# Kernel tuning notes

Hardware: AMD Instinct MI355X
Metric: run time of the kernel (lower is better)

Reference implementation:

```python
import jax, jax.numpy as jnp
import numpy as np

NUM_HEADS = 8
DIM = 384
KSIZE = 9  # res_kernel_size


def _moe_fc(x2d, gate_w, gate_b, w0, b0, w1, b1):
    # NaiveGate with top_k=1: softmax over a single top-1 logit == 1.0, so the
    # SparseDispatcher dispatch/exp/mul/log combine reduces exactly to selecting
    # the argmax expert's output per token.
    logits = x2d @ gate_w + gate_b                      # [T, 2]
    sel = jnp.argmax(logits, axis=-1)[:, None]          # [T, 1]
    y0 = x2d @ w0.T + b0
    y1 = x2d @ w1.T + b1
    return jnp.where(sel == 0, y0, y1)


def _forward(x, qkv_gate_w, qkv_gate_b, qkv_w0, qkv_w1,
             proj_gate_w, proj_gate_b, proj_w0, proj_b0, proj_w1, proj_b1,
             dconv_w):
    B, N, C = x.shape
    h, hd = NUM_HEADS, C // NUM_HEADS
    xt = x.reshape(-1, C)
    zero3 = jnp.zeros((3 * C,), x.dtype)  # qkv_bias=False
    qkv = _moe_fc(xt, qkv_gate_w, qkv_gate_b, qkv_w0, zero3, qkv_w1, zero3)
    qkv = qkv.reshape(B, N, 3, h, hd).transpose(2, 0, 3, 1, 4)  # [3,B,h,N,d]
    q, k, v = qkv[0], qkv[1], qkv[2]

    q = q / jnp.linalg.norm(q, axis=-1, keepdims=True)
    k = k / jnp.linalg.norm(k, axis=-1, keepdims=True)
    scale1 = jnp.mean(jnp.abs(q))
    scale2 = jnp.mean(jnp.abs(k))
    # straight-through binarization: fwd value = (x>0)*scale, grad flows via clamp(x,0,1)
    cq = jnp.clip(q, 0.0, 1.0)
    q = jax.lax.stop_gradient((q > 0).astype(q.dtype) * scale1 - cq) + cq
    ck = jnp.clip(k, 0.0, 1.0)
    k = jax.lax.stop_gradient((k > 0).astype(k.dtype) * scale2 - ck) + ck

    # depthwise residual conv over the token axis: v is [B, h, N, d], kernel (9,1)
    dconv_v = jax.lax.conv_general_dilated(
        v, dconv_w, window_strides=(1, 1), padding=[(KSIZE // 2, KSIZE // 2), (0, 0)],
        feature_group_count=h, dimension_numbers=("NCHW", "OIHW", "NCHW"))

    # linear-attention reorder: (K^T V) first -> O(N d^2)
    attn = jnp.einsum("bhnd,bhne->bhde", k, v)          # [B,h,d,d]
    out = 0.5 * v - (1.0 / jnp.pi) * jnp.einsum("bhnd,bhde->bhne", q, attn)
    out = out / jnp.linalg.norm(out, axis=-1, keepdims=True)
    out = out + dconv_v
    out = out.transpose(0, 2, 1, 3).reshape(B, N, C)

    out = _moe_fc(out.reshape(-1, C), proj_gate_w, proj_gate_b,
                  proj_w0, proj_b0, proj_w1, proj_b1)
    return out.reshape(B, N, C)


def setup_inputs() -> dict:
    key = jax.random.key(0)
    ks = jax.random.split(key, 12)
    B, N, C = 8, 4096, DIM
    s = 0.02
    return {
        "x": jax.random.normal(ks[0], (B, N, C), jnp.float32),
        "H": 64,
        "W": 64,
        "qkv_gate_w": jax.random.normal(ks[1], (C, 2), jnp.float32) * s,
        "qkv_gate_b": jnp.zeros((2,), jnp.float32),
        "qkv_w0": jax.random.normal(ks[2], (3 * C, C), jnp.float32) * s,
        "qkv_w1": jax.random.normal(ks[3], (3 * C, C), jnp.float32) * s,
        "proj_gate_w": jax.random.normal(ks[4], (C, 2), jnp.float32) * s,
        "proj_gate_b": jnp.zeros((2,), jnp.float32),
        "proj_w0": jax.random.normal(ks[5], (C, C), jnp.float32) * s,
        "proj_b0": jnp.zeros((C,), jnp.float32),
        "proj_w1": jax.random.normal(ks[6], (C, C), jnp.float32) * s,
        "proj_b1": jnp.zeros((C,), jnp.float32),
        "dconv_w": jax.random.normal(ks[7], (NUM_HEADS, 1, KSIZE, 1), jnp.float32) * s,
    }


def reference(x, H, W, qkv_gate_w, qkv_gate_b, qkv_w0, qkv_w1,
              proj_gate_w, proj_gate_b, proj_w0, proj_b0, proj_w1, proj_b1,
              dconv_w):
    # H, W are unused by the math (kept for signature fidelity)
    return _forward(x, qkv_gate_w, qkv_gate_b, qkv_w0, qkv_w1,
                    proj_gate_w, proj_gate_b, proj_w0, proj_b0, proj_w1, proj_b1,
                    dconv_w)
```

## Files before the change

### kernel.cpp

```cpp
#include <hip/hip_runtime.h>
#include <hip/hip_bf16.h>

#define BB 8
#define NN 4096
#define CC 384
#define HH 8
#define DD 48
#define TT (BB*NN)
#define CAP (TT + 128)
#define NROWT (CAP/128)
#define NQ ((size_t)BB*HH*NN*DD)
#define LISTCAP 32768

static_assert(CAP % 128 == 0, "cap");

typedef __attribute__((ext_vector_type(8))) short bf16x8;
typedef __attribute__((ext_vector_type(4))) float f32x4;

__device__ __forceinline__ float waveRedSum(float v){
  #pragma unroll
  for (int o = 32; o > 0; o >>= 1) v += __shfl_xor(v, o);
  return v;
}

__device__ __forceinline__ unsigned short f2bf(float f){
  unsigned u = __float_as_uint(f);
  u += 0x7FFFu + ((u >> 16) & 1u);
  return (unsigned short)(u >> 16);
}
__device__ __forceinline__ float bf2f(unsigned short h){
  return __uint_as_float(((unsigned)h) << 16);
}

__global__ void k_setup(const float* __restrict__ qw0, const float* __restrict__ qw1,
                        const float* __restrict__ pw0, const float* __restrict__ pw1,
                        unsigned short* __restrict__ qw0h, unsigned short* __restrict__ qw0l,
                        unsigned short* __restrict__ qw1h, unsigned short* __restrict__ qw1l,
                        unsigned short* __restrict__ pw0h, unsigned short* __restrict__ pw0l,
                        unsigned short* __restrict__ pw1h, unsigned short* __restrict__ pw1l,
                        int* __restrict__ perm0, int* __restrict__ perm1, int* __restrict__ cur){
  const int NQW = 1152*384/4, NPW = 384*384/4;
  if (blockIdx.x >= 1152){
    int i = (blockIdx.x - 1152)*256 + threadIdx.x;
    if (i < 8) cur[i] = 0;
    if (i < CAP){ perm0[i] = -1; perm1[i] = -1; }
    return;
  }
  int i = blockIdx.x*256 + threadIdx.x;
  const float* src; unsigned short* hi; unsigned short* lo; int off;
  if (i < NQW){ src = qw0; hi = qw0h; lo = qw0l; off = i; }
  else if (i < 2*NQW){ src = qw1; hi = qw1h; lo = qw1l; off = i - NQW; }
  else if (i < 2*NQW + NPW){ src = pw0; hi = pw0h; lo = pw0l; off = i - 2*NQW; }
  else if (i < 2*NQW + 2*NPW){ src = pw1; hi = pw1h; lo = pw1l; off = i - 2*NQW - NPW; }
  else return;
  float4 v = ((const float4*)src)[off];
  float f[4] = {v.x, v.y, v.z, v.w};
  unsigned short h[4], l[4];
  #pragma unroll
  for (int j = 0; j < 4; j++){
    h[j] = f2bf(f[j]);
    l[j] = f2bf(f[j] - bf2f(h[j]));
  }
  uint2 hv, lv;
  hv.x = h[0] | ((unsigned)h[1] << 16); hv.y = h[2] | ((unsigned)h[3] << 16);
  lv.x = l[0] | ((unsigned)l[1] << 16); lv.y = l[2] | ((unsigned)l[3] << 16);
  ((uint2*)hi)[off] = hv;
  ((uint2*)lo)[off] = lv;
}

__global__ void k_gate_scatter(const float* __restrict__ X,
                               const float* __restrict__ gw, const float* __restrict__ gb,
                               int* __restrict__ perm, int* __restrict__ cur,
                               unsigned char* __restrict__ selb,
                               unsigned short* __restrict__ Xhi, unsigned short* __restrict__ Xlo){
  const int lane = threadIdx.x & 63;
  const int wave = threadIdx.x >> 6;
  float gd[6];
  #pragma unroll
  for (int j = 0; j < 6; j++){
    int c = lane + 64*j;
    gd[j] = gw[c*2+1] - gw[c*2];
  }
  const float gbd = gb[1] - gb[0];
  const int tok0 = (blockIdx.x*4 + wave) * 32;
  unsigned mask = 0u;
  for (int i = 0; i < 32; i++){
    const size_t rowoff = (size_t)(tok0 + i) * CC;
    const float* xr = X + rowoff;
    float d = 0.f;
    #pragma unroll
    for (int j = 0; j < 6; j++){
      float xv = xr[lane + 64*j];
      d = fmaf(xv, gd[j], d);
      unsigned short h = f2bf(xv);
      Xhi[rowoff + lane + 64*j] = h;
      Xlo[rowoff + lane + 64*j] = f2bf(xv - bf2f(h));
    }
    d = waveRedSum(d);
    if (d + gbd > 0.f) mask |= (1u << i);
  }
  int n1 = __popc(mask), n0 = 32 - n1;
  int b0 = 0, b1 = 0;
  if (lane == 0){
    b0 = atomicAdd(cur + 0, n0);
    b1 = atomicAdd(cur + 1, n1);
  }
  b0 = __shfl(b0, 0); b1 = __shfl(b1, 0);
  if (lane < 32){
    int sel = (mask >> lane) & 1;
    unsigned below = mask & ((1u << lane) - 1u);
    int r1 = __popc(below);
    int r0 = lane - r1;
    int idx = sel ? (CAP - 1 - (b1 + r1)) : (b0 + r0);
    perm[idx] = tok0 + lane;
    selb[tok0 + lane] = (unsigned char)sel;
  }
}

__global__ void k_gate2(const float* __restrict__ gpart, const float* __restrict__ gb,
                        int* __restrict__ perm, int* __restrict__ cur){
  const int t = blockIdx.x*256 + threadIdx.x;
  const int lane = threadIdx.x & 63;
  const float gbd = gb[1] - gb[0];
  float4 a = ((const float4*)(gpart + (size_t)t*8))[0];
  float4 c = ((const float4*)(gpart + (size_t)t*8))[1];
  float d = ((a.x + a.y) + (a.z + a.w)) + ((c.x + c.y) + (c.z + c.w)) + gbd;
  bool sel = d > 0.f;
  unsigned long long m = __ballot(sel);
  int n1 = (int)__popcll(m);
  int b0 = 0, b1 = 0;
  if (lane == 0){
    b0 = atomicAdd(cur + 0, 64 - n1);
    b1 = atomicAdd(cur + 1, n1);
  }
  b0 = __shfl(b0, 0); b1 = __shfl(b1, 0);
  unsigned long long below = m & ((1ull << lane) - 1ull);
  int r1 = (int)__popcll(below);
  int r0 = lane - r1;
  int idx = sel ? (CAP - 1 - (b1 + r1)) : (b0 + r0);
  perm[idx] = t;
}

template<int NCOLS, int PASSES, bool IS_QKV>
__global__ __launch_bounds__(256, 2)
void k_gemm_mfma(const unsigned short* __restrict__ Ahi_g, const unsigned short* __restrict__ Alo_g,
                 const unsigned short* __restrict__ W0h, const unsigned short* __restrict__ W0l,
                 const unsigned short* __restrict__ W1h, const unsigned short* __restrict__ W1l,
                 const float* __restrict__ bias0, const float* __restrict__ bias1,
                 const int* __restrict__ perm, const int* __restrict__ cur,
                 unsigned short* __restrict__ oq, unsigned short* __restrict__ ok,
                 float* __restrict__ ov, float* __restrict__ oproj,
                 int* __restrict__ tlist, int* __restrict__ tcnt)
{
  constexpr int GDX = NCOLS / 128;
  constexpr int NWG = GDX * NROWT;
  constexpr int NB = (PASSES == 3) ? 2 : 1;
  __shared__ unsigned short As[NB][128*32];
  __shared__ unsigned short Bs[NB][128*32];
  __shared__ int permv[128];

  int orig = blockIdx.y * GDX + blockIdx.x;
  constexpr int qq = NWG >> 3, rr = NWG & 7;
  int xcd = orig & 7, slot = orig >> 3;
  int logical = (xcd < rr) ? (xcd*(qq+1) + slot) : (rr*(qq+1) + (xcd-rr)*qq + slot);
  const int bx = logical % GDX, by = logical / GDX;

  const int tid = threadIdx.x;
  const int m0 = by * 128, n0 = bx * 128;
  if (tid < 128) permv[tid] = perm[m0 + tid];
  __syncthreads();
  const int expert = (m0 > cur[0]) ? 1 : 0;
  const unsigned short* Wh = expert ? W1h : W0h;
  const unsigned short* Wl = expert ? W1l : W0l;

  const int c0 = tid, c1 = tid + 256;
  const int r0 = c0 >> 2, r1 = c1 >> 2;
  const int s0 = (((c0 & 3) ^ ((r0 >> 1) & 3))) * 8;
  const int s1 = (((c1 & 3) ^ ((r1 >> 1) & 3))) * 8;
  int t0 = permv[r0]; if (t0 < 0) t0 = 0;
  int t1 = permv[r1]; if (t1 < 0) t1 = 0;
  const unsigned short* a0h = Ahi_g + (size_t)t0*CC + s0;
  const unsigned short* a1h = Ahi_g + (size_t)t1*CC + s1;
  const unsigned short* b0h = Wh + (size_t)(n0 + r0)*CC + s0;
  const unsigned short* b1h = Wh + (size_t)(n0 + r1)*CC + s1;
  const unsigned short* a0l = nullptr; const unsigned short* a1l = nullptr;
  const unsigned short* b0l = nullptr; const unsigned short* b1l = nullptr;
  if constexpr (PASSES == 3){
    a0l = Alo_g + (size_t)t0*CC + s0;
    a1l = Alo_g + (size_t)t1*CC + s1;
    b0l = Wl + (size_t)(n0 + r0)*CC + s0;
    b1l = Wl + (size_t)(n0 + r1)*CC + s1;
  }
  const int d0 = c0*8, d1 = c1*8;

  const int lane = tid & 63;
  const int wv = tid >> 6, wr = wv >> 1, wc2 = wv & 1;
  const int lr = lane & 15, lg = lane >> 4;

  f32x4 acc[4][4];
  #pragma unroll
  for (int i = 0; i < 4; i++)
    #pragma unroll
    for (int j = 0; j < 4; j++) acc[i][j] = (f32x4){0.f, 0.f, 0.f, 0.f};

  int aoff[4], boff[4];
  #pragma unroll
  for (int f = 0; f < 4; f++){
    int ra = wr*64 + f*16 + lr;
    aoff[f] = ra*32 + ((lg ^ ((ra >> 1) & 3)) * 8);
    int rb = wc2*64 + f*16 + lr;
    boff[f] = rb*32 + ((lg ^ ((rb >> 1) & 3)) * 8);
  }

  #define GLD(gp, lp) __builtin_amdgcn_global_load_lds( \
      (const __attribute__((address_space(1))) void*)(gp), \
      (__attribute__((address_space(3))) void*)(lp), 16, 0, 0)

  for (int ko = 0; ko < CC; ko += 32){
    GLD(a0h + ko, &As[0][d0]);
    GLD(a1h + ko, &As[0][d1]);
    GLD(b0h + ko, &Bs[0][d0]);
    GLD(b1h + ko, &Bs[0][d1]);
    if constexpr (PASSES == 3){
      GLD(a0l + ko, &As[1][d0]);
      GLD(a1l + ko, &As[1][d1]);
      GLD(b0l + ko, &Bs[1][d0]);
      GLD(b1l + ko, &Bs[1][d1]);
    }
    __syncthreads();
    bf16x8 ah[4], bh[4], al[4], bl[4];
    #pragma unroll
    for (int f = 0; f < 4; f++){
      ah[f] = *(const bf16x8*)&As[0][aoff[f]];
      bh[f] = *(const bf16x8*)&Bs[0][boff[f]];
      if constexpr (PASSES == 3){
        al[f] = *(const bf16x8*)&As[1][aoff[f]];
        bl[f] = *(const bf16x8*)&Bs[1][boff[f]];
      }
    }
    #pragma unroll
    for (int mf = 0; mf < 4; mf++)
      #pragma unroll
      for (int nf = 0; nf < 4; nf++){
        acc[mf][nf] = __builtin_amdgcn_mfma_f32_16x16x32_bf16(ah[mf], bh[nf], acc[mf][nf], 0, 0, 0);
        if constexpr (PASSES == 3){
          acc[mf][nf] = __builtin_amdgcn_mfma_f32_16x16x32_bf16(al[mf], bh[nf], acc[mf][nf], 0, 0, 0);
          acc[mf][nf] = __builtin_amdgcn_mfma_f32_16x16x32_bf16(ah[mf], bl[nf], acc[mf][nf], 0, 0, 0);
        }
      }
    __syncthreads();
  }
  #undef GLD

  #pragma unroll
  for (int mf = 0; mf < 4; mf++){
    #pragma unroll
    for (int j = 0; j < 4; j++){
      const int rl = wr*64 + mf*16 + lg*4 + j;
      const int t = permv[rl];
      if (t < 0) continue;
      const int b = t >> 12, nn = t & 4095;
      #pragma unroll
      for (int nf = 0; nf < 4; nf++){
        const int col = n0 + wc2*64 + nf*16 + lr;
        const float val = acc[mf][nf][j];
        if constexpr (IS_QKV){
          const int which = col / CC;
          const int rem = col - which*CC;
          const int h = rem / DD;
          const int e = rem - h*DD;
          const size_t off = (((size_t)b*HH + h)*NN + nn)*DD + e;
          if (which == 0){
            oq[off] = f2bf(val);
            if (fabsf(val) < 2.5e-5f){
              int pq = atomicAdd(tcnt, 1);
              if (pq < LISTCAP) tlist[pq] = (int)off;
            }
          } else if (which == 1){
            ok[off] = f2bf(val);
            if (fabsf(val) < 2.5e-5f){
              int pq = atomicAdd(tcnt, 1);
              if (pq < LISTCAP) tlist[pq] = (int)(off + NQ);
            }
          } else {
            ov[off] = val;
          }
        } else {
          const float* bs = expert ? bias1 : bias0;
          oproj[(size_t)t*CC + col] = val + bs[col];
        }
      }
    }
  }
}

__global__ void k_topup_scales(unsigned short* __restrict__ qb, unsigned short* __restrict__ kb,
                               const int* __restrict__ list, const int* __restrict__ cnt,
                               const float* __restrict__ x,
                               const float* __restrict__ w0, const float* __restrict__ w1,
                               const unsigned char* __restrict__ selb,
                               float* __restrict__ part){
  __shared__ float sq[256], sk[256];
  if (blockIdx.x < 64){
    const int lane = threadIdx.x & 63;
    const int gw = (blockIdx.x*256 + threadIdx.x) >> 6;
    const int nwaves = 64 * 4;
    int n = cnt[0]; if (n > LISTCAP) n = LISTCAP;
    for (int e = gw; e < n; e += nwaves){
      int idx = list[e];
      int isK = (idx >= (int)NQ);
      int li = isK ? idx - (int)NQ : idx;
      int d = li % DD; int rest = li / DD;
      int nn = rest & 4095; int bh = rest >> 12;
      int b = bh >> 3, h = bh & 7;
      int t = b*NN + nn;
      int col = (isK ? CC : 0) + h*DD + d;
      const float* w = selb[t] ? w1 : w0;
      const float* xr = x + (size_t)t*CC;
      const float* wr = w + (size_t)col*CC;
      float s = 0.f;
      #pragma unroll
      for (int j = 0; j < 6; j++) s = fmaf(xr[lane + 64*j], wr[lane + 64*j], s);
      s = waveRedSum(s);
      if (lane == 0) (isK ? kb : qb)[li] = f2bf(s);
    }
    return;
  }
  const int blk = blockIdx.x - 64;
  const int row = blk*256 + threadIdx.x;
  const uint4* qp = (const uint4*)(qb + (size_t)row*DD);
  const uint4* kp = (const uint4*)(kb + (size_t)row*DD);
  float qss = 0.f, qsa = 0.f, kss = 0.f, ksa = 0.f;
  #pragma unroll
  for (int j = 0; j < 6; j++){
    uint4 u = qp[j];
    unsigned w[4] = {u.x, u.y, u.z, u.w};
    #pragma unroll
    for (int q2 = 0; q2 < 4; q2++){
      float f0 = bf2f((unsigned short)(w[q2] & 0xFFFFu));
      float f1 = bf2f((unsigned short)(w[q2] >> 16));
      qss = fmaf(f0, f0, qss); qsa += fabsf(f0);
      qss = fmaf(f1, f1, qss); qsa += fabsf(f1);
    }
    uint4 v = kp[j];
    unsigned w2[4] = {v.x, v.y, v.z, v.w};
    #pragma unroll
    for (int q2 = 0; q2 < 4; q2++){
      float f0 = bf2f((unsigned short)(w2[q2] & 0xFFFFu));
      float f1 = bf2f((unsigned short)(w2[q2] >> 16));
      kss = fmaf(f0, f0, kss); ksa += fabsf(f0);
      kss = fmaf(f1, f1, kss); ksa += fabsf(f1);
    }
  }
  sq[threadIdx.x] = qsa / sqrtf(qss);
  sk[threadIdx.x] = ksa / sqrtf(kss);
  __syncthreads();
  for (int s = 128; s > 0; s >>= 1){
    if (threadIdx.x < s){ sq[threadIdx.x] += sq[threadIdx.x+s]; sk[threadIdx.x] += sk[threadIdx.x+s]; }
    __syncthreads();
  }
  if (threadIdx.x == 0){
    part[blk*2+0] = sq[0];
    part[blk*2+1] = sk[0];
  }
}

__global__ void k_sred_attnp(const float* __restrict__ part_in, float* __restrict__ scalesb,
                             const unsigned short* __restrict__ kb, const float* __restrict__ vb,
                             float* __restrict__ part_out){
  if (blockIdx.x == 0){
    __shared__ float sq[256], sk[256];
    const int t = threadIdx.x;
    float aq = 0.f, ak = 0.f;
    for (int i = t; i < 1024; i += 256){ aq += part_in[2*i]; ak += part_in[2*i+1]; }
    sq[t] = aq; sk[t] = ak;
    __syncthreads();
    for (int s = 128; s > 0; s >>= 1){
      if (t < s){ sq[t] += sq[t+s]; sk[t] += sk[t+s]; }
      __syncthreads();
    }
    if (t == 0){
      scalesb[0] = sq[0] * (1.0f/12582912.0f);
      scalesb[1] = sk[0] * (1.0f/12582912.0f);
    }
    return;
  }
  __shared__ float ks[64][48];
  __shared__ float vs[64][48];
  const int idx = blockIdx.x - 1;
  const int bh = idx & 63, seg = idx >> 6;
  const int tid = threadIdx.x;
  const int ti = tid >> 5;
  const int tj = (tid >> 2) & 7;
  const int sl = tid & 3;
  const int dd0 = ti*6, ee0 = tj*6;
  const unsigned short* kbase = kb + ((size_t)bh*NN + seg*512) * DD;
  const float* vbase = vb + ((size_t)bh*NN + seg*512) * DD;
  float acc[6][6] = {};
  for (int c = 0; c < 8; c++){
    __syncthreads();
    for (int f = tid*2; f < 3072; f += 512){
      unsigned kk2 = *(const unsigned*)(kbase + c*3072 + f);
      float2 vv2 = *(const float2*)(vbase + c*3072 + f);
      (&ks[0][0])[f]   = ((short)(unsigned short)(kk2 & 0xFFFFu) > 0) ? 1.f : 0.f;
      (&ks[0][0])[f+1] = ((short)(unsigned short)(kk2 >> 16) > 0) ? 1.f : 0.f;
      (&vs[0][0])[f]   = vv2.x;
      (&vs[0][0])[f+1] = vv2.y;
    }
    __syncthreads();
    for (int nl = sl*16; nl < sl*16 + 16; nl++){
      float kk[6], vv[6];
      #pragma unroll
      for (int i = 0; i < 6; i++){ kk[i] = ks[nl][dd0+i]; vv[i] = vs[nl][ee0+i]; }
      #pragma unroll
      for (int i = 0; i < 6; i++)
        #pragma unroll
        for (int j = 0; j < 6; j++)
          acc[i][j] = fmaf(kk[i], vv[j], acc[i][j]);
    }
  }
  float* p = part_out + ((size_t)seg*64 + bh) * (DD*DD);
  #pragma unroll
  for (int i = 0; i < 6; i++)
    #pragma unroll
    for (int j = 0; j < 6; j++){
      float a = acc[i][j];
      a += __shfl_xor(a, 1);
      a += __shfl_xor(a, 2);
      if (sl == 0) p[(dd0+i)*48 + (ee0+j)] = a;
    }
}

__global__ void k_attn_reduce(const float* __restrict__ part, const float* __restrict__ scalesb,
                              unsigned short* __restrict__ aTh, unsigned short* __restrict__ aTl){
  const int bh = blockIdx.x;
  const float s2 = scalesb[1];
  for (int f = threadIdx.x; f < 3072; f += 256){
    const int e = f >> 6, d = f & 63;
    float s = 0.f;
    if (d < 48){
      #pragma unroll
      for (int seg = 0; seg < 8; seg++) s += part[((size_t)seg*64 + bh)*2304 + d*48 + e];
      s *= s2;
    }
    unsigned short hi = f2bf(s);
    aTh[(size_t)bh*3072 + f] = hi;
    aTl[(size_t)bh*3072 + f] = f2bf(s - bf2f(hi));
  }
}

__global__ __launch_bounds__(256, 4)
void k_fused(const unsigned short* __restrict__ qb, const float* __restrict__ vb,
             const unsigned short* __restrict__ aTh, const unsigned short* __restrict__ aTl,
             const float* __restrict__ scalesb, const float* __restrict__ dw,
             const float* __restrict__ pgw,
             unsigned short* __restrict__ intermh, float* __restrict__ gpart){
  __shared__ unsigned short aT[2][48*72];
  __shared__ float S_lds[128*48];
  __shared__ float wc[16];
  const int chunk = blockIdx.x;
  const int bh = blockIdx.y;
  const int b = bh >> 3, h = bh & 7;
  const int tid = threadIdx.x;
  const int lane = tid & 63, w = tid >> 6;
  const int lr = lane & 15, lg = lane >> 4;

  for (int idx = tid; idx < 384; idx += 256){
    const int e = idx >> 3, sl = idx & 7;
    *(uint4*)&aT[0][e*72 + sl*8] = *(const uint4*)(aTh + (size_t)bh*3072 + e*64 + sl*8);
    *(uint4*)&aT[1][e*72 + sl*8] = *(const uint4*)(aTl + (size_t)bh*3072 + e*64 + sl*8);
  }
  if (tid < 9) wc[tid] = dw[h*9 + tid];
  __syncthreads();

  bf16x8 afr[2][2];
  #pragma unroll
  for (int m = 0; m < 2; m++){
    #pragma unroll
    for (int ks = 0; ks < 2; ks++){
      const int d0 = ks*32 + lg*8;
      bf16x8 a = (bf16x8){0,0,0,0,0,0,0,0};
      if (d0 < 48){
        const int tok = chunk*128 + (w*2+m)*16 + lr;
        uint4 raw = *(const uint4*)(qb + ((size_t)bh*NN + tok)*DD + d0);
        unsigned wd[4] = {raw.x, raw.y, raw.z, raw.w};
        #pragma unroll
        for (int i2 = 0; i2 < 8; i2++){
          unsigned short el = (unsigned short)((wd[i2 >> 1] >> ((i2 & 1)*16)) & 0xFFFFu);
          a[i2] = ((short)el > 0) ? (short)0x3F80 : (short)0;
        }
      }
      afr[m][ks] = a;
    }
  }
  f32x4 acc[2][3];
  #pragma unroll
  for (int m = 0; m < 2; m++)
    #pragma unroll
    for (int nf = 0; nf < 3; nf++) acc[m][nf] = (f32x4){0.f,0.f,0.f,0.f};
  #pragma unroll
  for (int nf = 0; nf < 3; nf++){
    bf16x8 bhv[2], blv[2];
    #pragma unroll
    for (int ks = 0; ks < 2; ks++){
      const int bo = (nf*16 + lr)*72 + ks*32 + lg*8;
      bhv[ks] = *(const bf16x8*)&aT[0][bo];
      blv[ks] = *(const bf16x8*)&aT[1][bo];
    }
    #pragma unroll
    for (int m = 0; m < 2; m++)
      #pragma unroll
      for (int ks = 0; ks < 2; ks++){
        acc[m][nf] = __builtin_amdgcn_mfma_f32_16x16x32_bf16(afr[m][ks], bhv[ks], acc[m][nf], 0, 0, 0);
        acc[m][nf] = __builtin_amdgcn_mfma_f32_16x16x32_bf16(afr[m][ks], blv[ks], acc[m][nf], 0, 0, 0);
      }
  }
  #pragma unroll
  for (int m = 0; m < 2; m++)
    #pragma unroll
    for (int nf = 0; nf < 3; nf++)
      #pragma unroll
      for (int j = 0; j < 4; j++)
        S_lds[((w*2+m)*16 + lg*4 + j)*48 + nf*16 + lr] = acc[m][nf][j];
  __syncthreads();

  const float coef = scalesb[0] * 0.31830988618379067f;
  const float gdh = (lane < 48) ? (pgw[(h*48+lane)*2+1] - pgw[(h*48+lane)*2]) : 0.f;
  const float* vrow = vb + (size_t)bh*NN*DD;
  const int n0 = chunk*128 + w*32;
  float ring[9];
  #pragma unroll
  for (int k2 = 0; k2 < 8; k2++){
    int nn2 = n0 - 4 + k2;
    ring[k2] = (nn2 >= 0 && nn2 < NN && lane < 48) ? vrow[(size_t)nn2*DD + lane] : 0.f;
  }
  for (int it = 0; it < 32; it++){
    const int n = n0 + it;
    const int nh = n + 4;
    ring[8] = (nh < NN && lane < 48) ? vrow[(size_t)nh*DD + lane] : 0.f;
    const float vv = ring[4];
    const float Sv = (lane < 48) ? S_lds[(w*32 + it)*48 + lane] : 0.f;
    float op = 0.5f*vv - coef*Sv;
    float ss = waveRedSum(op*op);
    float res = op / sqrtf(ss);
    float dc = 0.f;
    #pragma unroll
    for (int k2 = 0; k2 < 9; k2++) dc = fmaf(wc[k2], ring[k2], dc);
    float r = res + dc;
    if (lane < 48)
      intermh[((size_t)b*NN + n)*CC + h*DD + lane] = f2bf(r);
    float gp = waveRedSum(r*gdh);
    if (lane == 0) gpart[((size_t)b*NN + n)*8 + h] = gp;
    #pragma unroll
    for (int k2 = 0; k2 < 8; k2++) ring[k2] = ring[k2+1];
  }
}

extern "C" void kernel_launch(void* const* d_in, const int* in_sizes, int n_in,
                              void* d_out, int out_size, void* d_ws, size_t ws_size,
                              hipStream_t stream){
  const float* x    = (const float*)d_in[0];
  const float* qgw  = (const float*)d_in[3];
  const float* qgb  = (const float*)d_in[4];
  const float* qw0  = (const float*)d_in[5];
  const float* qw1  = (const float*)d_in[6];
  const float* pgw  = (const float*)d_in[7];
  const float* pgb  = (const float*)d_in[8];
  const float* pw0  = (const float*)d_in[9];
  const float* pb0  = (const float*)d_in[10];
  const float* pw1  = (const float*)d_in[11];
  const float* pb1  = (const float*)d_in[12];
  const float* dw   = (const float*)d_in[13];
  float* out = (float*)d_out;

  char* p = (char*)d_ws;
  auto alloc = [&](size_t bytes){ char* r = p; p += (bytes + 255) & ~(size_t)255; return r; };

  unsigned short* qbuf = (unsigned short*)alloc(2*NQ);
  unsigned short* kbuf = (unsigned short*)alloc(2*NQ);
  float* vbuf          = (float*)alloc(4*NQ);
  char* xreg           = alloc(4*NQ);
  unsigned short* Xhi  = (unsigned short*)xreg;
  unsigned short* Xlo  = Xhi + NQ;
  unsigned short* intermh = (unsigned short*)xreg;
  unsigned short* qw0h = (unsigned short*)alloc(2*1152*384);
  unsigned short* qw0l = (unsigned short*)alloc(2*1152*384);
  unsigned short* qw1h = (unsigned short*)alloc(2*1152*384);
  unsigned short* qw1l = (unsigned short*)alloc(2*1152*384);
  unsigned short* pw0h = (unsigned short*)alloc(2*384*384);
  unsigned short* pw0l = (unsigned short*)alloc(2*384*384);
  unsigned short* pw1h = (unsigned short*)alloc(2*384*384);
  unsigned short* pw1l = (unsigned short*)alloc(2*384*384);
  float* attn_part     = (float*)alloc(4*(size_t)8*64*2304);
  unsigned short* aTh  = (unsigned short*)alloc(2*(size_t)64*3072);
  unsigned short* aTl  = (unsigned short*)alloc(2*(size_t)64*3072);
  float* scale_part    = (float*)alloc(4*2048);
  float* scalesb       = (float*)alloc(64);
  float* gpart         = (float*)alloc(4*(size_t)TT*8);
  int* perm_qkv        = (int*)alloc(4*CAP);
  int* perm_proj       = (int*)alloc(4*CAP);
  int* cur             = (int*)alloc(64);
  int* list            = (int*)alloc(4*LISTCAP);
  unsigned char* selq  = (unsigned char*)alloc(TT);

  k_setup<<<1152 + (CAP + 255)/256, 256, 0, stream>>>(
      qw0, qw1, pw0, pw1,
      qw0h, qw0l, qw1h, qw1l, pw0h, pw0l, pw1h, pw1l,
      perm_qkv, perm_proj, cur);

  k_gate_scatter<<<256, 256, 0, stream>>>(x, qgw, qgb, perm_qkv, cur, selq, Xhi, Xlo);

  {
    dim3 g(9, NROWT);
    k_gemm_mfma<1152, 3, true><<<g, 256, 0, stream>>>(
        Xhi, Xlo, qw0h, qw0l, qw1h, qw1l, nullptr, nullptr,
        perm_qkv, cur, qbuf, kbuf, vbuf, nullptr, list, cur + 4);
  }

  k_topup_scales<<<64 + 1024, 256, 0, stream>>>(qbuf, kbuf, list, cur + 4,
                                                x, qw0, qw1, selq, scale_part);

  k_sred_attnp<<<1 + 512, 256, 0, stream>>>(scale_part, scalesb, kbuf, vbuf, attn_part);

  k_attn_reduce<<<64, 256, 0, stream>>>(attn_part, scalesb, aTh, aTl);

  {
    dim3 g(32, 64);
    k_fused<<<g, 256, 0, stream>>>(qbuf, vbuf, aTh, aTl, scalesb, dw, pgw, intermh, gpart);
  }

  k_gate2<<<TT/256, 256, 0, stream>>>(gpart, pgb, perm_proj, cur + 2);

  {
    dim3 g(3, NROWT);
    k_gemm_mfma<384, 1, false><<<g, 256, 0, stream>>>(
        intermh, nullptr, pw0h, pw0l, pw1h, pw1l, pb0, pb1,
        perm_proj, cur + 2, nullptr, nullptr, nullptr, out, nullptr, nullptr);
  }
}
```

Before: 360.0 us.

## Load bf16 low-part GEMM fragments directly from global into registers

In the 3-pass split-bf16 MFMA GEMM, the low-part A and B tiles are now read straight from global memory into per-wave register fragments instead of being staged through LDS. This halves the shared-memory footprint and drops the 2-blocks-per-CU launch-bound hint. Each wave now loads its own low fragments with no sharing across waves, so redundant global/L2 traffic rises. The loads are also issued without a prefetch that would hide their latency.

```diff
diff --git a/kernel.cpp b/kernel.cpp
--- a/kernel.cpp
+++ b/kernel.cpp
@@ -142,7 +142,7 @@
 }
 
 template<int NCOLS, int PASSES, bool IS_QKV>
-__global__ __launch_bounds__(256, 2)
+__global__ __launch_bounds__(256)
 void k_gemm_mfma(const unsigned short* __restrict__ Ahi_g, const unsigned short* __restrict__ Alo_g,
                  const unsigned short* __restrict__ W0h, const unsigned short* __restrict__ W0l,
                  const unsigned short* __restrict__ W1h, const unsigned short* __restrict__ W1l,
@@ -154,9 +154,8 @@
 {
   constexpr int GDX = NCOLS / 128;
   constexpr int NWG = GDX * NROWT;
-  constexpr int NB = (PASSES == 3) ? 2 : 1;
-  __shared__ unsigned short As[NB][128*32];
-  __shared__ unsigned short Bs[NB][128*32];
+  __shared__ unsigned short As[128*32];
+  __shared__ unsigned short Bs[128*32];
   __shared__ int permv[128];
 
   int orig = blockIdx.y * GDX + blockIdx.x;
@@ -183,19 +182,22 @@
   const unsigned short* a1h = Ahi_g + (size_t)t1*CC + s1;
   const unsigned short* b0h = Wh + (size_t)(n0 + r0)*CC + s0;
   const unsigned short* b1h = Wh + (size_t)(n0 + r1)*CC + s1;
-  const unsigned short* a0l = nullptr; const unsigned short* a1l = nullptr;
-  const unsigned short* b0l = nullptr; const unsigned short* b1l = nullptr;
-  if constexpr (PASSES == 3){
-    a0l = Alo_g + (size_t)t0*CC + s0;
-    a1l = Alo_g + (size_t)t1*CC + s1;
-    b0l = Wl + (size_t)(n0 + r0)*CC + s0;
-    b1l = Wl + (size_t)(n0 + r1)*CC + s1;
-  }
   const int d0 = c0*8, d1 = c1*8;
 
   const int lane = tid & 63;
   const int wv = tid >> 6, wr = wv >> 1, wc2 = wv & 1;
   const int lr = lane & 15, lg = lane >> 4;
+
+  const unsigned short* aloP[4];
+  const unsigned short* bloP[4];
+  if constexpr (PASSES == 3){
+    #pragma unroll
+    for (int f = 0; f < 4; f++){
+      int tr = permv[wr*64 + f*16 + lr]; if (tr < 0) tr = 0;
+      aloP[f] = Alo_g + (size_t)tr*CC + lg*8;
+      bloP[f] = Wl + (size_t)(n0 + wc2*64 + f*16 + lr)*CC + lg*8;
+    }
+  }
 
   f32x4 acc[4][4];
   #pragma unroll
@@ -217,26 +219,24 @@
       (__attribute__((address_space(3))) void*)(lp), 16, 0, 0)
 
   for (int ko = 0; ko < CC; ko += 32){
-    GLD(a0h + ko, &As[0][d0]);
-    GLD(a1h + ko, &As[0][d1]);
-    GLD(b0h + ko, &Bs[0][d0]);
-    GLD(b1h + ko, &Bs[0][d1]);
+    bf16x8 al[4], bl[4];
     if constexpr (PASSES == 3){
-      GLD(a0l + ko, &As[1][d0]);
-      GLD(a1l + ko, &As[1][d1]);
-      GLD(b0l + ko, &Bs[1][d0]);
-      GLD(b1l + ko, &Bs[1][d1]);
-    }
+      #pragma unroll
+      for (int f = 0; f < 4; f++){
+        al[f] = *(const bf16x8*)(aloP[f] + ko);
+        bl[f] = *(const bf16x8*)(bloP[f] + ko);
+      }
+    }
+    GLD(a0h + ko, &As[d0]);
+    GLD(a1h + ko, &As[d1]);
+    GLD(b0h + ko, &Bs[d0]);
+    GLD(b1h + ko, &Bs[d1]);
     __syncthreads();
-    bf16x8 ah[4], bh[4], al[4], bl[4];
+    bf16x8 ah[4], bh[4];
     #pragma unroll
     for (int f = 0; f < 4; f++){
-      ah[f] = *(const bf16x8*)&As[0][aoff[f]];
-      bh[f] = *(const bf16x8*)&Bs[0][boff[f]];
-      if constexpr (PASSES == 3){
-        al[f] = *(const bf16x8*)&As[1][aoff[f]];
-        bl[f] = *(const bf16x8*)&Bs[1][boff[f]];
-      }
+      ah[f] = *(const bf16x8*)&As[aoff[f]];
+      bh[f] = *(const bf16x8*)&Bs[boff[f]];
     }
     #pragma unroll
     for (int mf = 0; mf < 4; mf++)
```

Result: slower. 433.6 us (+20.4%).
